# Kernel tuning notes

Hardware: AMD Instinct MI355X
Metric: run time of the kernel (lower is better)

The kernel has to match this reference:

```python
import jax, jax.numpy as jnp
import numpy as np

NUM_CLASSES = 80
NUM_CONVS = 4
SCORE_T = 0.05
TOPK = 1000
NMS_T = 0.6
MAX_DET = 100
STRIDES = (8, 16, 32, 64, 128)
LVL_HW = ((128, 168), (64, 84), (32, 42), (16, 21), (8, 11))
IMG_H, IMG_W = 1024, 1344
SCALE_CLAMP = float(np.log(1000.0 / 16.0))


def _conv(x, w, b):
    # x: (N,C,H,W), w: (O,I,3,3) -> same-padded 3x3 conv
    y = jax.lax.conv_general_dilated(x, w, (1, 1), 'SAME',
                                     dimension_numbers=('NCHW', 'OIHW', 'NCHW'))
    return y + b[None, :, None, None]


def _anchors(h, w, stride):
    # one anchor per location, size 4*stride, centered at pixel centers
    ys = (jnp.arange(h, dtype=jnp.float32) + 0.5) * stride
    xs = (jnp.arange(w, dtype=jnp.float32) + 0.5) * stride
    cy, cx = jnp.meshgrid(ys, xs, indexing='ij')
    cx, cy = cx.reshape(-1), cy.reshape(-1)
    half = 2.0 * stride
    return jnp.stack([cx - half, cy - half, cx + half, cy + half], -1)  # (HW,4)


def _decode(anchors, deltas):
    # Box2BoxTransform.apply_deltas with weights (1,1,1,1) + clip to image
    wa = anchors[..., 2] - anchors[..., 0]
    ha = anchors[..., 3] - anchors[..., 1]
    cxa = anchors[..., 0] + 0.5 * wa
    cya = anchors[..., 1] + 0.5 * ha
    dx, dy, dw, dh = (deltas[..., i] for i in range(4))
    dw = jnp.minimum(dw, SCALE_CLAMP)
    dh = jnp.minimum(dh, SCALE_CLAMP)
    cx = dx * wa + cxa
    cy = dy * ha + cya
    w = jnp.exp(dw) * wa
    h = jnp.exp(dh) * ha
    x1 = jnp.clip(cx - 0.5 * w, 0.0, IMG_W)
    y1 = jnp.clip(cy - 0.5 * h, 0.0, IMG_H)
    x2 = jnp.clip(cx + 0.5 * w, 0.0, IMG_W)
    y2 = jnp.clip(cy + 0.5 * h, 0.0, IMG_H)
    return jnp.stack([x1, y1, x2, y2], -1)


def _nms_single(boxes, scores, classes):
    # class-aware greedy NMS (batched_nms via per-class coordinate offset)
    M = boxes.shape[0]
    b = boxes + (classes.astype(boxes.dtype) * 2000.0)[:, None]
    order = jnp.argsort(-scores)
    b = b[order]
    s = scores[order]
    areas = (b[:, 2] - b[:, 0]) * (b[:, 3] - b[:, 1])
    idx = jnp.arange(M)

    def body(i, keep):
        bi = b[i]
        xx1 = jnp.maximum(bi[0], b[:, 0])
        yy1 = jnp.maximum(bi[1], b[:, 1])
        xx2 = jnp.minimum(bi[2], b[:, 2])
        yy2 = jnp.minimum(bi[3], b[:, 3])
        inter = jnp.clip(xx2 - xx1, 0.0) * jnp.clip(yy2 - yy1, 0.0)
        iou = inter / (areas[i] + areas - inter + 1e-9)
        sup = (iou > NMS_T) & (idx > i)
        alive = keep[i] & (s[i] > 0)
        return jnp.where(alive, keep & ~sup, keep)

    keep = jax.lax.fori_loop(0, M, body, jnp.ones((M,), bool))
    topv, topi = jax.lax.top_k(jnp.where(keep, s, 0.0), MAX_DET)
    sel = order[topi]
    return boxes[sel], topv, classes[sel]


def _forward(feat0, feat1, feat2, feat3, feat4, cls_w, cls_b, box_w, box_b,
             score_w, score_b, pred_w, pred_b, ctr_w, ctr_b):
    feats = [feat0, feat1, feat2, feat3, feat4]
    all_boxes, all_scores, all_classes = [], [], []
    for lvl, f in enumerate(feats):
        N = f.shape[0]
        x = f
        for i in range(NUM_CONVS):
            x = jax.nn.relu(_conv(x, cls_w[i], cls_b[i]))
        logits = _conv(x, score_w, score_b)          # (N,80,H,W)
        ctr = _conv(x, ctr_w, ctr_b)                 # (N,1,H,W)
        y = f
        for i in range(NUM_CONVS):
            y = jax.nn.relu(_conv(y, box_w[i], box_b[i]))
        deltas = _conv(y, pred_w, pred_b)            # (N,4,H,W)
        # permute_to_N_HWA_K
        logits = logits.transpose(0, 2, 3, 1).reshape(N, -1, NUM_CLASSES)
        deltas = deltas.transpose(0, 2, 3, 1).reshape(N, -1, 4)
        ctr = ctr.transpose(0, 2, 3, 1).reshape(N, -1, 1)
        scores = jnp.sqrt(jax.nn.sigmoid(logits) * jax.nn.sigmoid(ctr))
        flat = scores.reshape(N, -1)                 # (N, HW*K)
        k = min(TOPK, flat.shape[1])
        topv, topi = jax.lax.top_k(flat, k)
        topv = jnp.where(topv > SCORE_T, topv, 0.0)  # score threshold
        aidx = topi // NUM_CLASSES
        cidx = topi % NUM_CLASSES
        d = jnp.take_along_axis(deltas, aidx[..., None], axis=1)  # (N,k,4)
        h, w = LVL_HW[lvl]
        anc = _anchors(h, w, STRIDES[lvl])[aidx]     # (N,k,4)
        all_boxes.append(_decode(anc, d))
        all_scores.append(topv)
        all_classes.append(cidx)
    boxes = jnp.concatenate(all_boxes, 1)
    scores = jnp.concatenate(all_scores, 1)
    classes = jnp.concatenate(all_classes, 1)
    return jax.vmap(_nms_single)(boxes, scores, classes)


def setup_inputs() -> dict:
    key = jax.random.key(0)
    ks = jax.random.split(key, 10)
    d = {}
    shapes = {'feat0': (2, 256, 128, 168), 'feat1': (2, 256, 64, 84),
              'feat2': (2, 256, 32, 42), 'feat3': (2, 256, 16, 21),
              'feat4': (2, 256, 8, 11)}
    for i, (n, s) in enumerate(shapes.items()):
        d[n] = jax.random.normal(ks[i], s, dtype=jnp.float32)
    d['cls_w'] = jax.random.normal(ks[5], (4, 256, 256, 3, 3), jnp.float32) * 0.01
    d['cls_b'] = jnp.zeros((4, 256), jnp.float32)
    d['box_w'] = jax.random.normal(ks[6], (4, 256, 256, 3, 3), jnp.float32) * 0.01
    d['box_b'] = jnp.zeros((4, 256), jnp.float32)
    d['score_w'] = jax.random.normal(ks[7], (80, 256, 3, 3), jnp.float32) * 0.01
    d['score_b'] = jnp.full((80,), -float(np.log((1 - 0.01) / 0.01)), jnp.float32)
    d['pred_w'] = jax.random.normal(ks[8], (4, 256, 3, 3), jnp.float32) * 0.01
    d['pred_b'] = jnp.zeros((4,), jnp.float32)
    d['ctr_w'] = jax.random.normal(ks[9], (1, 256, 3, 3), jnp.float32) * 0.01
    d['ctr_b'] = jnp.zeros((1,), jnp.float32)
    return d


def reference(feat0, feat1, feat2, feat3, feat4, cls_w, cls_b, box_w, box_b,
              score_w, score_b, pred_w, pred_b, ctr_w, ctr_b):
    # returns (pred_boxes (N,100,4), scores (N,100), pred_classes (N,100))
    return _forward(feat0, feat1, feat2, feat3, feat4, cls_w, cls_b, box_w,
                    box_b, score_w, score_b, pred_w, pred_b, ctr_w, ctr_b)
```

## Files before the change

kernel.cpp:

```cpp
#include <hip/hip_runtime.h>
#include <math.h>

#define NCLS 80
#define KTOP 1000
#define SCORE_T 0.05f
#define NMS_T 0.6f
#define SCALE_CLAMP 4.135166556742356f
#define IMGW 1344.0f
#define IMGH 1024.0f

struct MCfg {
    const float* feat[5];
    long offIn[5];
    long offOutA[5];
    long offOutB[5];
    int tileBase[6];
    int tilesX[5];
    int Hs[5];
    int Ws[5];
    int nLvl;
    int useFeats;
};

template<int RELU>
__global__ __launch_bounds__(256, 2)
void conv_g(MCfg cfg,
            const float* __restrict__ inA, const float* __restrict__ inB,
            const float* __restrict__ wA, const float* __restrict__ wB,
            const float* __restrict__ bA, const float* __restrict__ bB,
            float* __restrict__ outA, float* __restrict__ outB,
            int CoutA, int CoutB, int zA)
{
    __shared__ float sIn[2][8][10][20];
    const int tid = threadIdx.x;
    const int n   = blockIdx.y;
    const int z   = blockIdx.z;
    const bool isA = (z < zA);
    const float* wt   = isA ? wA : wB;
    const float* bias = isA ? bA : bB;
    const int Cout    = isA ? CoutA : CoutB;
    const int cout0   = (isA ? z : z - zA) * 64;

    int tile = blockIdx.x;
    int lvl = 0;
    while (lvl + 1 < cfg.nLvl && tile >= cfg.tileBase[lvl + 1]) ++lvl;
    int t = tile - cfg.tileBase[lvl];
    const int tX = cfg.tilesX[lvl];
    int ty = 0;
    while (t >= tX) { t -= tX; ++ty; }
    const int tx = t;
    const int H = cfg.Hs[lvl], W = cfg.Ws[lvl], HW = H * W;
    const float* inbase = cfg.useFeats ? cfg.feat[lvl]
                                       : ((isA ? inA : inB) + cfg.offIn[lvl]);
    const float* inN = inbase + (size_t)n * 256 * HW;
    float* outbase = isA ? (outA + cfg.offOutA[lvl]) : (outB + cfg.offOutB[lvl]);

    const int h0 = ty * 8, w0 = tx * 16;
    const int cell = tid & 15, cg = tid >> 4;
    const int pr = (cell >> 2) << 1;
    const int pc = (cell & 3) << 2;
    const int q = tid & 3, pp0 = tid >> 2;

    float acc[4][8];
#pragma unroll
    for (int a = 0; a < 4; ++a)
#pragma unroll
        for (int b = 0; b < 8; ++b) acc[a][b] = 0.f;

    float rIn[10];

    auto issue = [&](int ci0) {
#pragma unroll
        for (int it = 0; it < 2; ++it) {
            int p = pp0 + it * 64;
            if (p < 80) {
                int ci = p / 10, row = p - ci * 10;
                int gh = h0 + row - 1;
                const float* src = inN + (size_t)(ci0 + ci) * HW;
#pragma unroll
                for (int j = 0; j < 5; ++j) {
                    int col = q * 5 + j, gw = w0 + col - 1;
                    float v = 0.f;
                    if (col < 18 && (unsigned)gh < (unsigned)H && (unsigned)gw < (unsigned)W)
                        v = src[(long)gh * W + gw];
                    rIn[it * 5 + j] = v;
                }
            }
        }
    };
    auto commit = [&](int buf) {
#pragma unroll
        for (int it = 0; it < 2; ++it) {
            int p = pp0 + it * 64;
            if (p < 80) {
                int ci = p / 10, row = p - ci * 10;
#pragma unroll
                for (int j = 0; j < 5; ++j)
                    sIn[buf][ci][row][q * 5 + j] = rIn[it * 5 + j];
            }
        }
    };

    const int cout_my = cout0 + cg * 4;

    issue(0);
    commit(0);
    __syncthreads();

    for (int r = 0; r < 32; ++r) {
        if (r < 31) issue((r + 1) * 8);
        const int cur = r & 1;
        const int cibase = r * 8;
#pragma unroll 2
        for (int ci = 0; ci < 8; ++ci) {
            float x[4][6];
#pragma unroll
            for (int rr = 0; rr < 4; ++rr)
#pragma unroll
                for (int c = 0; c < 6; ++c) x[rr][c] = sIn[cur][ci][pr + rr][pc + c];
#pragma unroll
            for (int cc = 0; cc < 4; ++cc) {
                int gc = cout_my + cc;
                int gcw = (gc < Cout) ? gc : 0;
                const float* wp = wt + ((size_t)gcw * 256 + (cibase + ci)) * 9;
                float4 wa = *(const float4*)(wp);
                float4 wb = *(const float4*)(wp + 4);
                float w8 = wp[8];
                float wv[9] = { wa.x, wa.y, wa.z, wa.w, wb.x, wb.y, wb.z, wb.w, w8 };
#pragma unroll
                for (int py = 0; py < 2; ++py)
#pragma unroll
                    for (int px = 0; px < 4; ++px) {
                        float s = acc[cc][py * 4 + px];
#pragma unroll
                        for (int dy = 0; dy < 3; ++dy)
#pragma unroll
                            for (int dx = 0; dx < 3; ++dx)
                                s = fmaf(wv[dy * 3 + dx], x[py + dy][px + dx], s);
                        acc[cc][py * 4 + px] = s;
                    }
            }
        }
        if (r < 31) commit((r + 1) & 1);
        __syncthreads();
    }

#pragma unroll
    for (int cc = 0; cc < 4; ++cc) {
        int gc = cout_my + cc;
        if (gc >= Cout) continue;
        float b = bias[gc];
        float* outc = outbase + ((size_t)n * Cout + gc) * HW;
#pragma unroll
        for (int py = 0; py < 2; ++py) {
            int gh = h0 + pr + py;
            if (gh >= H) continue;
#pragma unroll
            for (int px = 0; px < 4; ++px) {
                int gw = w0 + pc + px;
                if (gw >= W) continue;
                float v = acc[cc][py * 4 + px] + b;
                if (RELU) v = fmaxf(v, 0.f);
                outc[gh * W + gw] = v;
            }
        }
    }
}

__global__ void pack_kernel(const float* __restrict__ sw, const float* __restrict__ sb,
                            const float* __restrict__ cw, const float* __restrict__ cb,
                            float* __restrict__ pw, float* __restrict__ pb)
{
    int i = blockIdx.x * 256 + threadIdx.x;
    const int tot = 81 * 2304;
    if (i < tot) pw[i] = (i < 80 * 2304) ? sw[i] : cw[i - 80 * 2304];
    if (i < 81)  pb[i] = (i < 80) ? sb[i] : cb[i - 80];
}

struct LvlT {
    int HW[5]; int W[5]; float stride[5];
    long off81[5]; long offD[5];
};

__device__ inline float score_at(const float* __restrict__ L, int HW, int c, int pos)
{
    float l = L[(size_t)c * HW + pos];
    float ct = L[(size_t)80 * HW + pos];
    float sl = 1.f / (1.f + expf(-l));
    float sc = 1.f / (1.f + expf(-ct));
    return sqrtf(sl * sc);
}

__global__ __launch_bounds__(256)
void hist_b(LvlT T, const float* __restrict__ lg, unsigned* __restrict__ hist,
            const int* __restrict__ sel, int pass)
{
    __shared__ unsigned h[4096];
    int n = blockIdx.y, lvl = blockIdx.z, g = lvl * 2 + n;
    int HW = T.HW[lvl];
    int nel = HW * 80;
    const float* L = lg + T.off81[lvl] + (size_t)n * 81 * HW;
    unsigned* Hh = hist + g * 4096;
    const int* SL = sel + g * 8;
    for (int i = threadIdx.x; i < 4096; i += 256) h[i] = 0;
    __syncthreads();
    unsigned b1 = 0, b2 = 0;
    if (pass >= 1) b1 = (unsigned)SL[0];
    if (pass == 2) b2 = (unsigned)SL[2];
    int stride = gridDim.x * 256;
    for (int i = blockIdx.x * 256 + threadIdx.x; i < nel; i += stride) {
        int c = i / HW, pos = i - c * HW;
        unsigned bits = __float_as_uint(score_at(L, HW, c, pos));
        if (pass == 0) atomicAdd(&h[bits >> 24], 1u);
        else if (pass == 1) { if ((bits >> 24) == b1) atomicAdd(&h[(bits >> 12) & 0xFFFu], 1u); }
        else { if ((bits >> 12) == ((b1 << 12) | b2)) atomicAdd(&h[bits & 0xFFFu], 1u); }
    }
    __syncthreads();
    for (int i = threadIdx.x; i < 4096; i += 256)
        if (h[i]) atomicAdd(&Hh[i], h[i]);
}

__global__ __launch_bounds__(1024)
void scan_b(const unsigned* __restrict__ hist, int* __restrict__ sel, int pass)
{
    __shared__ unsigned ps[1024];
    int g = blockIdx.x;
    const unsigned* H = hist + g * 4096;
    int* SL = sel + g * 8;
    int tid = threadIdx.x;
    unsigned s = 0;
    if (pass == 0) s = (tid < 256) ? H[tid] : 0u;
    else { for (int b = 0; b < 4; ++b) s += H[tid * 4 + b]; }
    ps[tid] = s;
    __syncthreads();
    if (tid == 0) {
        unsigned base = 0;
        if (pass == 1) base = (unsigned)SL[1];
        else if (pass == 2) base = (unsigned)SL[3];
        unsigned cum = base, prev = 0;
        int fb = -1;
        for (int t = 1023; t >= 0; --t) {
            if (cum + ps[t] >= (unsigned)KTOP) {
                if (pass == 0) { fb = t; prev = cum; }
                else {
                    for (int b = t * 4 + 3; b >= t * 4; --b) {
                        unsigned c = H[b];
                        if (cum + c >= (unsigned)KTOP) { fb = b; prev = cum; break; }
                        cum += c;
                    }
                }
                break;
            }
            cum += ps[t];
        }
        if (pass == 0) { SL[0] = fb; SL[1] = (int)prev; }
        else if (pass == 1) { SL[2] = fb; SL[3] = (int)prev; }
        else {
            unsigned T = (((unsigned)SL[0]) << 24) | (((unsigned)SL[2]) << 12) | (unsigned)fb;
            SL[4] = (int)T; SL[5] = KTOP - (int)prev; SL[6] = (int)prev;
        }
    }
}

__global__ __launch_bounds__(256)
void compact_b(LvlT T, const float* __restrict__ lg, const int* __restrict__ sel,
               int* __restrict__ candIdx, float* __restrict__ candScore,
               unsigned* __restrict__ eqList, int* __restrict__ counters)
{
    int n = blockIdx.y, lvl = blockIdx.z, g = lvl * 2 + n;
    int HW = T.HW[lvl];
    int nel = HW * 80;
    const float* L = lg + T.off81[lvl] + (size_t)n * 81 * HW;
    unsigned Tt = (unsigned)sel[g * 8 + 4];
    int* cnt = counters + g * 2;
    int stride = gridDim.x * 256;
    for (int i = blockIdx.x * 256 + threadIdx.x; i < nel; i += stride) {
        int c = i / HW, pos = i - c * HW;
        float v = score_at(L, HW, c, pos);
        unsigned bits = __float_as_uint(v);
        int flat = pos * 80 + c;
        if (bits > Tt) {
            int s = atomicAdd(&cnt[0], 1);
            if (s < KTOP) {
                candIdx[n * 5000 + lvl * 1000 + s] = flat;
                candScore[n * 5000 + lvl * 1000 + s] = v;
            }
        } else if (bits == Tt) {
            int e = atomicAdd(&cnt[1], 1);
            if (e < 4096) eqList[g * 4096 + e] = (unsigned)flat;
        }
    }
}

template<typename T>
__device__ inline void bitonicSort(T* a, int N, bool desc)
{
    for (int k = 2; k <= N; k <<= 1)
        for (int j = k >> 1; j >= 1; j >>= 1) {
            for (int i = threadIdx.x; i < N; i += blockDim.x) {
                int l = i ^ j;
                if (l > i) {
                    T x = a[i], y = a[l];
                    bool up = ((i & k) == 0);
                    bool sw = desc ? (up ? (x < y) : (x > y)) : (up ? (x > y) : (x < y));
                    if (sw) { a[i] = y; a[l] = x; }
                }
            }
            __syncthreads();
        }
}

__global__ __launch_bounds__(256)
void eqfinish_b(const unsigned* __restrict__ eqList, const int* __restrict__ sel,
                const int* __restrict__ counters, int* __restrict__ candIdx,
                float* __restrict__ candScore)
{
    __shared__ unsigned L[4096];
    int g = blockIdx.x;
    int lvl = g >> 1, n = g & 1;
    int e = counters[g * 2 + 1]; if (e > 4096) e = 4096;
    int needEq = sel[g * 8 + 5];
    int base = sel[g * 8 + 6];
    unsigned T = (unsigned)sel[g * 8 + 4];
    for (int i = threadIdx.x; i < 4096; i += 256) L[i] = (i < e) ? eqList[g * 4096 + i] : 0xFFFFFFFFu;
    __syncthreads();
    bitonicSort(L, 4096, false);
    for (int t = threadIdx.x; t < needEq; t += 256) {
        int s = base + t;
        if (s < KTOP) {
            candIdx[n * 5000 + lvl * 1000 + s] = (int)L[t];
            candScore[n * 5000 + lvl * 1000 + s] = __uint_as_float(T);
        }
    }
}

__global__ __launch_bounds__(256)
void lvlsort_b(int* __restrict__ candIdx, float* __restrict__ candScore)
{
    __shared__ unsigned long long K[1024];
    int g = blockIdx.x;
    int lvl = g >> 1, n = g & 1;
    int* CI = candIdx + n * 5000 + lvl * 1000;
    float* CS = candScore + n * 5000 + lvl * 1000;
    for (int i = threadIdx.x; i < 1024; i += blockDim.x)
        K[i] = (i < KTOP)
             ? ((((unsigned long long)(unsigned)CI[i]) << 32) | __float_as_uint(CS[i]))
             : 0xFFFFFFFFFFFFFFFFULL;
    __syncthreads();
    bitonicSort(K, 1024, false);
    for (int i = threadIdx.x; i < KTOP; i += blockDim.x) {
        CI[i] = (int)(K[i] >> 32);
        CS[i] = __uint_as_float((unsigned)(K[i] & 0xFFFFFFFFu));
    }
}

__global__ __launch_bounds__(256)
void decode_b(LvlT T, const int* __restrict__ candIdx, const float* __restrict__ candScore,
              const float* __restrict__ deltas, float* __restrict__ candBox,
              float* __restrict__ candZ, int* __restrict__ candCls)
{
    int t = blockIdx.x * 256 + threadIdx.x;
    if (t >= 2 * 5000) return;
    int n = t / 5000, r = t % 5000;
    int lvl = r / 1000;
    int HW = T.HW[lvl], W = T.W[lvl];
    float stride = T.stride[lvl];
    int g = n * 5000 + r;
    int idx = candIdx[g];
    float raw = candScore[g];
    int pos = idx / NCLS, cls = idx % NCLS;
    int hh = pos / W, ww = pos % W;
    float cxa0 = ((float)ww + 0.5f) * stride;
    float cya0 = ((float)hh + 0.5f) * stride;
    float half = 2.f * stride;
    float a0 = cxa0 - half, a1 = cya0 - half, a2 = cxa0 + half, a3 = cya0 + half;
    float wa = a2 - a0, ha = a3 - a1;
    float cxa = a0 + 0.5f * wa, cya = a1 + 0.5f * ha;
    const float* D = deltas + T.offD[lvl] + (size_t)n * 4 * HW;
    float dx = D[pos], dy = D[HW + pos], dw = D[2 * HW + pos], dh = D[3 * HW + pos];
    dw = fminf(dw, SCALE_CLAMP); dh = fminf(dh, SCALE_CLAMP);
    float cx = dx * wa + cxa, cy = dy * ha + cya;
    float w2 = expf(dw) * wa, h2 = expf(dh) * ha;
    float x1 = fminf(fmaxf(cx - 0.5f * w2, 0.f), IMGW);
    float y1 = fminf(fmaxf(cy - 0.5f * h2, 0.f), IMGH);
    float x2 = fminf(fmaxf(cx + 0.5f * w2, 0.f), IMGW);
    float y2 = fminf(fmaxf(cy + 0.5f * h2, 0.f), IMGH);
    candBox[g * 4 + 0] = x1; candBox[g * 4 + 1] = y1;
    candBox[g * 4 + 2] = x2; candBox[g * 4 + 3] = y2;
    candZ[g] = (raw > SCORE_T) ? raw : 0.f;
    candCls[g] = cls;
}

__global__ __launch_bounds__(1024)
void gsort_kernel(const float* __restrict__ candZ, const float* __restrict__ candBox,
                  const int* __restrict__ candCls, float* __restrict__ sBox,
                  float* __restrict__ sScore, float* __restrict__ sCls,
                  float* __restrict__ sOffB, float* __restrict__ sArea)
{
    __shared__ unsigned long long K[8192];
    int n = blockIdx.x;
    for (int i = threadIdx.x; i < 8192; i += 1024)
        K[i] = (i < 5000)
             ? ((((unsigned long long)__float_as_uint(candZ[n * 5000 + i])) << 16)
                | (unsigned long long)(65535 - i))
             : 0ULL;
    __syncthreads();
    bitonicSort(K, 8192, true);
    for (int r = threadIdx.x; r < 5000; r += 1024) {
        unsigned long long k = K[r];
        int g = 65535 - (int)(k & 0xFFFFULL);
        float s = __uint_as_float((unsigned)((k >> 16) & 0xFFFFFFFFULL));
        int cls = candCls[n * 5000 + g];
        float b0 = candBox[(n * 5000 + g) * 4 + 0];
        float b1 = candBox[(n * 5000 + g) * 4 + 1];
        float b2 = candBox[(n * 5000 + g) * 4 + 2];
        float b3 = candBox[(n * 5000 + g) * 4 + 3];
        size_t o = (size_t)n * 5000 + r;
        sBox[o * 4 + 0] = b0; sBox[o * 4 + 1] = b1; sBox[o * 4 + 2] = b2; sBox[o * 4 + 3] = b3;
        sScore[o] = s;
        sCls[o] = (float)cls;
        float off = (float)cls * 2000.0f;
        float o0 = b0 + off, o1 = b1 + off, o2 = b2 + off, o3 = b3 + off;
        sOffB[o * 4 + 0] = o0; sOffB[o * 4 + 1] = o1; sOffB[o * 4 + 2] = o2; sOffB[o * 4 + 3] = o3;
        sArea[o] = (o2 - o0) * (o3 - o1);
    }
}

__global__ __launch_bounds__(64)
void nms_mask_kernel(const float* __restrict__ sOffB, const float* __restrict__ sArea,
                     unsigned long long* __restrict__ masks)
{
    __shared__ float jb0[64], jb1[64], jb2[64], jb3[64], ja[64];
    int jw = blockIdx.x;
    int it = blockIdx.y;
    int n  = blockIdx.z;
    int t = threadIdx.x;
    int jj = jw * 64 + t;
    const float* B = sOffB + (size_t)n * 5000 * 4;
    const float* A = sArea + (size_t)n * 5000;
    if (jj < 5000) {
        jb0[t] = B[jj * 4]; jb1[t] = B[jj * 4 + 1];
        jb2[t] = B[jj * 4 + 2]; jb3[t] = B[jj * 4 + 3];
        ja[t] = A[jj];
    } else {
        jb0[t] = -3e8f; jb1[t] = -3e8f; jb2[t] = -3e8f; jb3[t] = -3e8f; ja[t] = 0.f;
    }
    __syncthreads();
    int i = it * 64 + t;
    if (i >= 5000) return;
    float b0 = B[i * 4], b1 = B[i * 4 + 1], b2 = B[i * 4 + 2], b3 = B[i * 4 + 3];
    float ai = A[i];
    unsigned long long m = 0;
    for (int u = 0; u < 64; ++u) {
        float xx1 = fmaxf(b0, jb0[u]);
        float yy1 = fmaxf(b1, jb1[u]);
        float xx2 = fminf(b2, jb2[u]);
        float yy2 = fminf(b3, jb3[u]);
        float iw = fmaxf(xx2 - xx1, 0.f), ih = fmaxf(yy2 - yy1, 0.f);
        float inter = iw * ih;
        float iou = inter / (ai + ja[u] - inter + 1e-9f);
        if (iou > NMS_T) m |= (1ull << u);
    }
    masks[((size_t)n * 5000 + i) * 79 + jw] = m;
}

__global__ __launch_bounds__(128)
void nms_scan_kernel(const unsigned long long* __restrict__ masks,
                     const float* __restrict__ sScore, const float* __restrict__ sBox,
                     const float* __restrict__ sCls, float* __restrict__ out)
{
    __shared__ unsigned long long rem[80];
    __shared__ int alive[100], dead[100];
    __shared__ int st[3];
    int n = blockIdx.x, t = threadIdx.x;
    const float* S = sScore + (size_t)n * 5000;
    for (int i = t; i < 80; i += 128) rem[i] = 0ull;
    if (t == 0) { st[0] = 0; st[1] = 0; }
    __syncthreads();
    for (int i = 0; i < 5000; ++i) {
        if (t == 0) {
            bool sup = (rem[i >> 6] >> (i & 63)) & 1ull;
            float s = S[i];
            bool al = (!sup) && (s > 0.f);
            st[2] = al ? 1 : 0;
            if (al) { if (st[0] < 100) alive[st[0]] = i; st[0]++; }
            else    { if (st[1] < 100) dead[st[1]] = i;  st[1]++; }
        }
        __syncthreads();
        bool stop = (st[0] >= 100);
        if (st[2] && !stop) {
            const unsigned long long* row = masks + ((size_t)n * 5000 + i) * 79;
            if (t < 79) rem[t] |= row[t];
        }
        __syncthreads();
        if (stop) break;
    }
    __syncthreads();
    int na = st[0]; if (na > 100) na = 100;
    for (int r = t; r < 100; r += 128) {
        int p; float sc;
        if (r < na) { p = alive[r]; sc = S[p]; }
        else { p = dead[r - na]; sc = 0.f; }
        const float* bb = sBox + (((size_t)n * 5000) + p) * 4;
        out[(n * 100 + r) * 4 + 0] = bb[0];
        out[(n * 100 + r) * 4 + 1] = bb[1];
        out[(n * 100 + r) * 4 + 2] = bb[2];
        out[(n * 100 + r) * 4 + 3] = bb[3];
        out[800 + n * 100 + r] = sc;
        out[1000 + n * 100 + r] = sCls[(size_t)n * 5000 + p];
    }
}

extern "C" void kernel_launch(void* const* d_in, const int* in_sizes, int n_in,
                              void* d_out, int out_size, void* d_ws, size_t ws_size,
                              hipStream_t stream)
{
    const float* feat[5] = { (const float*)d_in[0], (const float*)d_in[1],
                             (const float*)d_in[2], (const float*)d_in[3],
                             (const float*)d_in[4] };
    const float* cls_w   = (const float*)d_in[5];
    const float* cls_b   = (const float*)d_in[6];
    const float* box_w   = (const float*)d_in[7];
    const float* box_b   = (const float*)d_in[8];
    const float* score_w = (const float*)d_in[9];
    const float* score_b = (const float*)d_in[10];
    const float* pred_w  = (const float*)d_in[11];
    const float* pred_b  = (const float*)d_in[12];
    const float* ctr_w   = (const float*)d_in[13];
    const float* ctr_b   = (const float*)d_in[14];

    char* ws = (char*)d_ws;
    size_t off = 0;
    auto alloc = [&](size_t nbytes) -> void* {
        void* p = ws + off;
        off += (nbytes + 255) & ~(size_t)255;
        return p;
    };
    const int   LH[5]  = { 128, 64, 32, 16, 8 };
    const int   LW[5]  = { 168, 84, 42, 21, 11 };
    const float LS[5]  = { 8.f, 16.f, 32.f, 64.f, 128.f };
    const int   LHW[5] = { 21504, 5376, 1344, 336, 88 };
    long off81[5], offD[5];
    { long a = 0, d = 0;
      for (int l = 0; l < 5; ++l) { off81[l] = a; offD[l] = d; a += 2L * 81 * LHW[l]; d += 2L * 4 * LHW[l]; } }
    long off256_14[4];
    { long a = 0; for (int l = 0; l < 4; ++l) { off256_14[l] = a; a += 2L * 256 * LHW[l + 1]; } }

    float* lg81   = (float*)alloc(sizeof(float) * (off81[4] + 2L * 81 * LHW[4]));
    float* deltas = (float*)alloc(sizeof(float) * (offD[4] + 2L * 4 * LHW[4]));
    float* packw  = (float*)alloc(sizeof(float) * 81 * 2304);
    float* packb  = (float*)alloc(sizeof(float) * 128);
    unsigned* hist = (unsigned*)alloc(sizeof(unsigned) * 10 * 4096);
    int* sel       = (int*)alloc(sizeof(int) * 10 * 8);
    int* counters  = (int*)alloc(sizeof(int) * 10 * 2);
    unsigned* eqList = (unsigned*)alloc(sizeof(unsigned) * 10 * 4096);
    int* candIdx     = (int*)alloc(sizeof(int) * 2 * 5000);
    float* candScore = (float*)alloc(sizeof(float) * 2 * 5000);
    float* candZ     = (float*)alloc(sizeof(float) * 2 * 5000);
    float* candBox   = (float*)alloc(sizeof(float) * 2 * 5000 * 4);
    int* candCls     = (int*)alloc(sizeof(int) * 2 * 5000);
    float* sBox   = (float*)alloc(sizeof(float) * 2 * 5000 * 4);
    float* sScore = (float*)alloc(sizeof(float) * 2 * 5000);
    float* sCls   = (float*)alloc(sizeof(float) * 2 * 5000);
    float* sOffB  = (float*)alloc(sizeof(float) * 2 * 5000 * 4);
    float* sArea  = (float*)alloc(sizeof(float) * 2 * 5000);

    const size_t bigE = 2L * 256 * LHW[0];
    const size_t bigB = sizeof(float) * bigE;
    bool wide = (ws_size >= off + 4 * (bigB + 256) + (1u << 20));

    float* clsP = (float*)alloc(bigB);
    float* clsQ = (float*)alloc(bigB);
    float* boxP = wide ? (float*)alloc(bigB) : clsP;
    float* boxQ = wide ? (float*)alloc(bigB) : clsQ;
    unsigned long long* masks = (unsigned long long*)clsP;

    pack_kernel<<<(81 * 2304 + 255) / 256, 256, 0, stream>>>(score_w, score_b, ctr_w, ctr_b, packw, packb);

    const size_t WS = 589824;

    MCfg c0{}, c0f{}, c0h{}, c14{}, c14f{}, c14h{};
    c0.feat[0] = feat[0];
    c0.tileBase[0] = 0; c0.tileBase[1] = 176;
    c0.tilesX[0] = 11; c0.Hs[0] = 128; c0.Ws[0] = 168;
    c0.nLvl = 1; c0.useFeats = 0;
    c0f = c0; c0f.useFeats = 1;
    c0h = c0;
    for (int l = 0; l < 4; ++l) {
        c14.feat[l] = feat[l + 1];
        c14.offIn[l] = off256_14[l];
        c14.offOutA[l] = off256_14[l];
        c14.offOutB[l] = off256_14[l];
        c14.tilesX[l] = (LW[l + 1] + 15) / 16;
        c14.Hs[l] = LH[l + 1]; c14.Ws[l] = LW[l + 1];
    }
    c14.tileBase[0] = 0; c14.tileBase[1] = 48; c14.tileBase[2] = 60;
    c14.tileBase[3] = 64; c14.tileBase[4] = 65;
    c14.nLvl = 4; c14.useFeats = 0;
    c14f = c14; c14f.useFeats = 1;
    c14h = c14;
    for (int l = 0; l < 4; ++l) { c14h.offOutA[l] = off81[l + 1]; c14h.offOutB[l] = offD[l + 1]; }

    if (wide) {
        dim3 gT(176, 2, 8), gH(176, 2, 3);
        conv_g<1><<<gT, 256, 0, stream>>>(c0f, feat[0], feat[0], cls_w + 0 * WS, box_w + 0 * WS, cls_b + 0,   box_b + 0,   clsP, boxP, 256, 256, 4);
        conv_g<1><<<gT, 256, 0, stream>>>(c0,  clsP,    boxP,    cls_w + 1 * WS, box_w + 1 * WS, cls_b + 256, box_b + 256, clsQ, boxQ, 256, 256, 4);
        conv_g<1><<<gT, 256, 0, stream>>>(c0,  clsQ,    boxQ,    cls_w + 2 * WS, box_w + 2 * WS, cls_b + 512, box_b + 512, clsP, boxP, 256, 256, 4);
        conv_g<1><<<gT, 256, 0, stream>>>(c0,  clsP,    boxP,    cls_w + 3 * WS, box_w + 3 * WS, cls_b + 768, box_b + 768, clsQ, boxQ, 256, 256, 4);
        conv_g<0><<<gH, 256, 0, stream>>>(c0h, clsQ,    boxQ,    packw,          pred_w,         packb,       pred_b,      lg81, deltas, 81, 4, 2);
        dim3 gT2(65, 2, 8), gH2(65, 2, 3);
        conv_g<1><<<gT2, 256, 0, stream>>>(c14f, feat[1], feat[1], cls_w + 0 * WS, box_w + 0 * WS, cls_b + 0,   box_b + 0,   clsP, boxP, 256, 256, 4);
        conv_g<1><<<gT2, 256, 0, stream>>>(c14,  clsP,    boxP,    cls_w + 1 * WS, box_w + 1 * WS, cls_b + 256, box_b + 256, clsQ, boxQ, 256, 256, 4);
        conv_g<1><<<gT2, 256, 0, stream>>>(c14,  clsQ,    boxQ,    cls_w + 2 * WS, box_w + 2 * WS, cls_b + 512, box_b + 512, clsP, boxP, 256, 256, 4);
        conv_g<1><<<gT2, 256, 0, stream>>>(c14,  clsP,    boxP,    cls_w + 3 * WS, box_w + 3 * WS, cls_b + 768, box_b + 768, clsQ, boxQ, 256, 256, 4);
        conv_g<0><<<gH2, 256, 0, stream>>>(c14h, clsQ,    boxQ,    packw,          pred_w,         packb,       pred_b,      lg81, deltas, 81, 4, 2);
    } else {
        dim3 gT(176, 2, 4), gHL(176, 2, 2), gHP(176, 2, 1);
        MCfg c0hL = c0, c0hP = c0;
        conv_g<1><<<gT, 256, 0, stream>>>(c0f, feat[0], feat[0], cls_w + 0 * WS, cls_w, cls_b + 0,   cls_b, clsP, clsP, 256, 256, 4);
        conv_g<1><<<gT, 256, 0, stream>>>(c0,  clsP,    clsP,    cls_w + 1 * WS, cls_w, cls_b + 256, cls_b, clsQ, clsQ, 256, 256, 4);
        conv_g<1><<<gT, 256, 0, stream>>>(c0,  clsQ,    clsQ,    cls_w + 2 * WS, cls_w, cls_b + 512, cls_b, clsP, clsP, 256, 256, 4);
        conv_g<1><<<gT, 256, 0, stream>>>(c0,  clsP,    clsP,    cls_w + 3 * WS, cls_w, cls_b + 768, cls_b, clsQ, clsQ, 256, 256, 4);
        conv_g<0><<<gHL, 256, 0, stream>>>(c0hL, clsQ,  clsQ,    packw,          packw, packb,       packb, lg81, lg81, 81, 81, 2);
        conv_g<1><<<gT, 256, 0, stream>>>(c0f, feat[0], feat[0], box_w + 0 * WS, box_w, box_b + 0,   box_b, clsP, clsP, 256, 256, 4);
        conv_g<1><<<gT, 256, 0, stream>>>(c0,  clsP,    clsP,    box_w + 1 * WS, box_w, box_b + 256, box_b, clsQ, clsQ, 256, 256, 4);
        conv_g<1><<<gT, 256, 0, stream>>>(c0,  clsQ,    clsQ,    box_w + 2 * WS, box_w, box_b + 512, box_b, clsP, clsP, 256, 256, 4);
        conv_g<1><<<gT, 256, 0, stream>>>(c0,  clsP,    clsP,    box_w + 3 * WS, box_w, box_b + 768, box_b, clsQ, clsQ, 256, 256, 4);
        conv_g<0><<<gHP, 256, 0, stream>>>(c0hP, clsQ,  clsQ,    pred_w,         pred_w, pred_b,     pred_b, deltas, deltas, 4, 4, 1);
        dim3 gT2(65, 2, 4), gHL2(65, 2, 2), gHP2(65, 2, 1);
        MCfg c14hL = c14h, c14hP = c14h;
        for (int l = 0; l < 4; ++l) { c14hP.offOutA[l] = offD[l + 1]; }
        conv_g<1><<<gT2, 256, 0, stream>>>(c14f, feat[1], feat[1], cls_w + 0 * WS, cls_w, cls_b + 0,   cls_b, clsP, clsP, 256, 256, 4);
        conv_g<1><<<gT2, 256, 0, stream>>>(c14,  clsP,    clsP,    cls_w + 1 * WS, cls_w, cls_b + 256, cls_b, clsQ, clsQ, 256, 256, 4);
        conv_g<1><<<gT2, 256, 0, stream>>>(c14,  clsQ,    clsQ,    cls_w + 2 * WS, cls_w, cls_b + 512, cls_b, clsP, clsP, 256, 256, 4);
        conv_g<1><<<gT2, 256, 0, stream>>>(c14,  clsP,    clsP,    cls_w + 3 * WS, cls_w, cls_b + 768, cls_b, clsQ, clsQ, 256, 256, 4);
        conv_g<0><<<gHL2, 256, 0, stream>>>(c14hL, clsQ, clsQ,    packw,          packw, packb,       packb, lg81, lg81, 81, 81, 2);
        conv_g<1><<<gT2, 256, 0, stream>>>(c14f, feat[1], feat[1], box_w + 0 * WS, box_w, box_b + 0,   box_b, clsP, clsP, 256, 256, 4);
        conv_g<1><<<gT2, 256, 0, stream>>>(c14,  clsP,    clsP,    box_w + 1 * WS, box_w, box_b + 256, box_b, clsQ, clsQ, 256, 256, 4);
        conv_g<1><<<gT2, 256, 0, stream>>>(c14,  clsQ,    clsQ,    box_w + 2 * WS, box_w, box_b + 512, box_b, clsP, clsP, 256, 256, 4);
        conv_g<1><<<gT2, 256, 0, stream>>>(c14,  clsP,    clsP,    box_w + 3 * WS, box_w, box_b + 768, box_b, clsQ, clsQ, 256, 256, 4);
        conv_g<0><<<gHP2, 256, 0, stream>>>(c14hP, clsQ, clsQ,    pred_w,         pred_w, pred_b,     pred_b, deltas, deltas, 4, 4, 1);
    }

    LvlT T{};
    for (int l = 0; l < 5; ++l) {
        T.HW[l] = LHW[l]; T.W[l] = LW[l]; T.stride[l] = LS[l];
        T.off81[l] = off81[l]; T.offD[l] = offD[l];
    }
    dim3 gHist(128, 2, 5);
    hipMemsetAsync(hist, 0, 10 * 4096 * sizeof(unsigned), stream);
    hist_b<<<gHist, 256, 0, stream>>>(T, lg81, hist, sel, 0);
    scan_b<<<10, 1024, 0, stream>>>(hist, sel, 0);
    hipMemsetAsync(hist, 0, 10 * 4096 * sizeof(unsigned), stream);
    hist_b<<<gHist, 256, 0, stream>>>(T, lg81, hist, sel, 1);
    scan_b<<<10, 1024, 0, stream>>>(hist, sel, 1);
    hipMemsetAsync(hist, 0, 10 * 4096 * sizeof(unsigned), stream);
    hist_b<<<gHist, 256, 0, stream>>>(T, lg81, hist, sel, 2);
    scan_b<<<10, 1024, 0, stream>>>(hist, sel, 2);
    hipMemsetAsync(counters, 0, 10 * 2 * sizeof(int), stream);
    compact_b<<<gHist, 256, 0, stream>>>(T, lg81, sel, candIdx, candScore, eqList, counters);
    eqfinish_b<<<10, 256, 0, stream>>>(eqList, sel, counters, candIdx, candScore);
    lvlsort_b<<<10, 256, 0, stream>>>(candIdx, candScore);
    decode_b<<<(2 * 5000 + 255) / 256, 256, 0, stream>>>(T, candIdx, candScore, deltas,
                                                         candBox, candZ, candCls);
    gsort_kernel<<<2, 1024, 0, stream>>>(candZ, candBox, candCls, sBox, sScore, sCls, sOffB, sArea);
    dim3 gM(79, 79, 2);
    nms_mask_kernel<<<gM, 64, 0, stream>>>(sOffB, sArea, masks);
    nms_scan_kernel<<<2, 128, 0, stream>>>(masks, sScore, sBox, sCls, (float*)d_out);
}
```

Baseline: 10.00 ms.

## Restructure 3x3 conv with wave-uniform packed weights, larger tiles and fused heads

Replaces the conv kernel with a variant that uses 16x16 spatial tiles and up to 1024 threads per block. Each wave owns four output channels, so its weight reads are wave-uniform (readfirstlane) and can come from scalar loads. Weights are repacked once into a 12-float-aligned layout so each tap group loads as two float4 plus one scalar. The class-logit, centerness and box-delta heads are merged into one packed 96-channel head launch. The aim is to cut per-lane weight traffic and launch count, at the cost of fewer accumulators per thread, a larger shared-memory footprint and an extra repack pass over the tower weights.

```diff
diff --git a/kernel.cpp b/kernel.cpp
--- a/kernel.cpp
+++ b/kernel.cpp
@@ -22,24 +22,23 @@
     int useFeats;
 };
 
-template<int RELU>
-__global__ __launch_bounds__(256, 2)
-void conv_g(MCfg cfg,
+template<int NW, int HEAD>
+__global__ __launch_bounds__(NW * 64)
+void conv_s(MCfg cfg,
             const float* __restrict__ inA, const float* __restrict__ inB,
-            const float* __restrict__ wA, const float* __restrict__ wB,
-            const float* __restrict__ bA, const float* __restrict__ bB,
-            float* __restrict__ outA, float* __restrict__ outB,
-            int CoutA, int CoutB, int zA)
-{
-    __shared__ float sIn[2][8][10][20];
+            const float* __restrict__ wpkA, const float* __restrict__ wpkB,
+            const float* __restrict__ biasA, const float* __restrict__ biasB,
+            float* __restrict__ outA, float* __restrict__ outB, int zA)
+{
+    __shared__ float sIn[2][8][18][20];
     const int tid = threadIdx.x;
     const int n   = blockIdx.y;
     const int z   = blockIdx.z;
     const bool isA = (z < zA);
-    const float* wt   = isA ? wA : wB;
-    const float* bias = isA ? bA : bB;
-    const int Cout    = isA ? CoutA : CoutB;
-    const int cout0   = (isA ? z : z - zA) * 64;
+    const float* wpk  = isA ? wpkA : wpkB;
+    const float* bias = isA ? biasA : biasB;
+    const int cbase = HEAD ? (isA ? z * 16 : 80)
+                           : (isA ? z : z - zA) * 64;
 
     int tile = blockIdx.x;
     int lvl = 0;
@@ -53,128 +52,174 @@
     const float* inbase = cfg.useFeats ? cfg.feat[lvl]
                                        : ((isA ? inA : inB) + cfg.offIn[lvl]);
     const float* inN = inbase + (size_t)n * 256 * HW;
-    float* outbase = isA ? (outA + cfg.offOutA[lvl]) : (outB + cfg.offOutB[lvl]);
-
-    const int h0 = ty * 8, w0 = tx * 16;
-    const int cell = tid & 15, cg = tid >> 4;
-    const int pr = (cell >> 2) << 1;
-    const int pc = (cell & 3) << 2;
-    const int q = tid & 3, pp0 = tid >> 2;
-
-    float acc[4][8];
+
+    const int h0 = ty * 16, w0 = tx * 16;
+    const int wv  = __builtin_amdgcn_readfirstlane(tid >> 6);
+    const int gc0 = cbase + wv * 4;
+    const float* wb = wpk + (size_t)gc0 * 3072;
+    const int lane = tid & 63;
+    const int pr = (lane >> 3) << 1;
+    const int pc = (lane & 7) << 1;
+
+    float acc[4][4];
 #pragma unroll
     for (int a = 0; a < 4; ++a)
 #pragma unroll
-        for (int b = 0; b < 8; ++b) acc[a][b] = 0.f;
-
-    float rIn[10];
+        for (int b = 0; b < 4; ++b) acc[a][b] = 0.f;
+
+    constexpr int NTHR = NW * 64;
+    constexpr int NIT = (2592 + NTHR - 1) / NTHR;
+    float rIn[NIT];
 
     auto issue = [&](int ci0) {
 #pragma unroll
-        for (int it = 0; it < 2; ++it) {
-            int p = pp0 + it * 64;
-            if (p < 80) {
-                int ci = p / 10, row = p - ci * 10;
-                int gh = h0 + row - 1;
-                const float* src = inN + (size_t)(ci0 + ci) * HW;
-#pragma unroll
-                for (int j = 0; j < 5; ++j) {
-                    int col = q * 5 + j, gw = w0 + col - 1;
-                    float v = 0.f;
-                    if (col < 18 && (unsigned)gh < (unsigned)H && (unsigned)gw < (unsigned)W)
-                        v = src[(long)gh * W + gw];
-                    rIn[it * 5 + j] = v;
-                }
+        for (int it = 0; it < NIT; ++it) {
+            int idx = it * NTHR + tid;
+            float v = 0.f;
+            if (idx < 2592) {
+                int ci = idx / 324, rm = idx - ci * 324;
+                int row = rm / 18, col = rm - row * 18;
+                int gh = h0 + row - 1, gw = w0 + col - 1;
+                if ((unsigned)gh < (unsigned)H && (unsigned)gw < (unsigned)W)
+                    v = inN[(size_t)(ci0 + ci) * HW + (long)gh * W + gw];
             }
+            rIn[it] = v;
         }
     };
     auto commit = [&](int buf) {
 #pragma unroll
-        for (int it = 0; it < 2; ++it) {
-            int p = pp0 + it * 64;
-            if (p < 80) {
-                int ci = p / 10, row = p - ci * 10;
-#pragma unroll
-                for (int j = 0; j < 5; ++j)
-                    sIn[buf][ci][row][q * 5 + j] = rIn[it * 5 + j];
+        for (int it = 0; it < NIT; ++it) {
+            int idx = it * NTHR + tid;
+            if (idx < 2592) {
+                int ci = idx / 324, rm = idx - ci * 324;
+                int row = rm / 18, col = rm - row * 18;
+                sIn[buf][ci][row][col] = rIn[it];
             }
         }
     };
-
-    const int cout_my = cout0 + cg * 4;
 
     issue(0);
     commit(0);
     __syncthreads();
 
-    for (int r = 0; r < 32; ++r) {
-        if (r < 31) issue((r + 1) * 8);
-        const int cur = r & 1;
-        const int cibase = r * 8;
-#pragma unroll 2
+    for (int rs = 0; rs < 32; ++rs) {
+        if (rs < 31) issue((rs + 1) * 8);
+        const float (*S)[18][20] = sIn[rs & 1];
+        const int cib = rs * 8;
+#pragma unroll
         for (int ci = 0; ci < 8; ++ci) {
-            float x[4][6];
-#pragma unroll
-            for (int rr = 0; rr < 4; ++rr)
-#pragma unroll
-                for (int c = 0; c < 6; ++c) x[rr][c] = sIn[cur][ci][pr + rr][pc + c];
+            float x[4][4];
+#pragma unroll
+            for (int i = 0; i < 4; ++i) {
+                float2 u0 = *(const float2*)&S[ci][pr + i][pc];
+                float2 u1 = *(const float2*)&S[ci][pr + i][pc + 2];
+                x[i][0] = u0.x; x[i][1] = u0.y; x[i][2] = u1.x; x[i][3] = u1.y;
+            }
 #pragma unroll
             for (int cc = 0; cc < 4; ++cc) {
-                int gc = cout_my + cc;
-                int gcw = (gc < Cout) ? gc : 0;
-                const float* wp = wt + ((size_t)gcw * 256 + (cibase + ci)) * 9;
-                float4 wa = *(const float4*)(wp);
-                float4 wb = *(const float4*)(wp + 4);
-                float w8 = wp[8];
-                float wv[9] = { wa.x, wa.y, wa.z, wa.w, wb.x, wb.y, wb.z, wb.w, w8 };
+                const float* wp = wb + cc * 3072 + (size_t)(cib + ci) * 12;
+                float4 qa = *(const float4*)wp;
+                float4 qb = *(const float4*)(wp + 4);
+                float q8 = wp[8];
+                float wv9[9] = { qa.x, qa.y, qa.z, qa.w, qb.x, qb.y, qb.z, qb.w, q8 };
 #pragma unroll
                 for (int py = 0; py < 2; ++py)
 #pragma unroll
-                    for (int px = 0; px < 4; ++px) {
-                        float s = acc[cc][py * 4 + px];
+                    for (int px = 0; px < 2; ++px) {
+                        float s = acc[cc][py * 2 + px];
 #pragma unroll
                         for (int dy = 0; dy < 3; ++dy)
 #pragma unroll
                             for (int dx = 0; dx < 3; ++dx)
-                                s = fmaf(wv[dy * 3 + dx], x[py + dy][px + dx], s);
-                        acc[cc][py * 4 + px] = s;
+                                s = fmaf(wv9[dy * 3 + dx], x[py + dy][px + dx], s);
+                        acc[cc][py * 2 + px] = s;
                     }
             }
         }
-        if (r < 31) commit((r + 1) & 1);
+        if (rs < 31) commit((rs + 1) & 1);
         __syncthreads();
     }
 
 #pragma unroll
     for (int cc = 0; cc < 4; ++cc) {
-        int gc = cout_my + cc;
-        if (gc >= Cout) continue;
+        int gc = gc0 + cc;
+        if (HEAD) {
+            if (isA) { if (gc >= 81) continue; }
+            else     { if (gc < 81 || gc >= 85) continue; }
+        }
         float b = bias[gc];
-        float* outc = outbase + ((size_t)n * Cout + gc) * HW;
+        float* outc;
+        if (!HEAD)
+            outc = (isA ? outA + cfg.offOutA[lvl] : outB + cfg.offOutB[lvl])
+                 + ((size_t)n * 256 + gc) * HW;
+        else if (isA)
+            outc = outA + cfg.offOutA[lvl] + ((size_t)n * 81 + gc) * HW;
+        else
+            outc = outB + cfg.offOutB[lvl] + ((size_t)n * 4 + (gc - 81)) * HW;
 #pragma unroll
         for (int py = 0; py < 2; ++py) {
             int gh = h0 + pr + py;
             if (gh >= H) continue;
 #pragma unroll
-            for (int px = 0; px < 4; ++px) {
+            for (int px = 0; px < 2; ++px) {
                 int gw = w0 + pc + px;
                 if (gw >= W) continue;
-                float v = acc[cc][py * 4 + px] + b;
-                if (RELU) v = fmaxf(v, 0.f);
-                outc[gh * W + gw] = v;
+                float v = acc[cc][py * 2 + px] + b;
+                if (!HEAD) v = fmaxf(v, 0.f);
+                outc[(long)gh * W + gw] = v;
             }
         }
     }
 }
 
-__global__ void pack_kernel(const float* __restrict__ sw, const float* __restrict__ sb,
-                            const float* __restrict__ cw, const float* __restrict__ cb,
-                            float* __restrict__ pw, float* __restrict__ pb)
-{
+__global__ __launch_bounds__(256)
+void packT_kernel(const float* __restrict__ cw, const float* __restrict__ bw,
+                  float* __restrict__ dst)
+{
+    const long tot = 2L * 4 * 256 * 256 * 12;
+    long stride = (long)gridDim.x * 256;
+    for (long i = (long)blockIdx.x * 256 + threadIdx.x; i < tot; i += stride) {
+        int k = (int)(i % 12);
+        long r = i / 12;
+        int ci = (int)(r % 256); r /= 256;
+        int co = (int)(r % 256); r /= 256;
+        int layer = (int)(r % 4);
+        int tower = (int)(r / 4);
+        const float* src = tower ? bw : cw;
+        float v = (k < 9) ? src[(((size_t)layer * 256 + co) * 256 + ci) * 9 + k] : 0.f;
+        dst[i] = v;
+    }
+}
+
+__global__ __launch_bounds__(256)
+void packH_kernel(const float* __restrict__ sw, const float* __restrict__ sb,
+                  const float* __restrict__ cw, const float* __restrict__ cb,
+                  const float* __restrict__ pw, const float* __restrict__ pb,
+                  float* __restrict__ dst, float* __restrict__ dstb)
+{
+    const int tot = 96 * 256 * 12;
+    int stride = gridDim.x * 256;
+    for (int i = blockIdx.x * 256 + threadIdx.x; i < tot; i += stride) {
+        int k = i % 12;
+        int r = i / 12;
+        int ci = r % 256;
+        int co = r / 256;
+        float v = 0.f;
+        if (k < 9) {
+            if (co < 80)      v = sw[((size_t)co * 256 + ci) * 9 + k];
+            else if (co == 80) v = cw[(size_t)ci * 9 + k];
+            else if (co < 85)  v = pw[((size_t)(co - 81) * 256 + ci) * 9 + k];
+        }
+        dst[i] = v;
+    }
     int i = blockIdx.x * 256 + threadIdx.x;
-    const int tot = 81 * 2304;
-    if (i < tot) pw[i] = (i < 80 * 2304) ? sw[i] : cw[i - 80 * 2304];
-    if (i < 81)  pb[i] = (i < 80) ? sb[i] : cb[i - 80];
+    if (i < 96) {
+        float v = 0.f;
+        if (i < 80) v = sb[i];
+        else if (i == 80) v = cb[0];
+        else if (i < 85) v = pb[i - 81];
+        dstb[i] = v;
+    }
 }
 
 struct LvlT {
@@ -546,10 +591,12 @@
     long off256_14[4];
     { long a = 0; for (int l = 0; l < 4; ++l) { off256_14[l] = a; a += 2L * 256 * LHW[l + 1]; } }
 
+    const long LSTRIDE = 256L * 256 * 12;
+    float* packT  = (float*)alloc(sizeof(float) * 2 * 4 * LSTRIDE);
+    float* packH  = (float*)alloc(sizeof(float) * 96 * 256 * 12);
+    float* packHb = (float*)alloc(sizeof(float) * 96);
     float* lg81   = (float*)alloc(sizeof(float) * (off81[4] + 2L * 81 * LHW[4]));
     float* deltas = (float*)alloc(sizeof(float) * (offD[4] + 2L * 4 * LHW[4]));
-    float* packw  = (float*)alloc(sizeof(float) * 81 * 2304);
-    float* packb  = (float*)alloc(sizeof(float) * 128);
     unsigned* hist = (unsigned*)alloc(sizeof(unsigned) * 10 * 4096);
     int* sel       = (int*)alloc(sizeof(int) * 10 * 8);
     int* counters  = (int*)alloc(sizeof(int) * 10 * 2);
@@ -565,9 +612,9 @@
     float* sOffB  = (float*)alloc(sizeof(float) * 2 * 5000 * 4);
     float* sArea  = (float*)alloc(sizeof(float) * 2 * 5000);
 
-    const size_t bigE = 2L * 256 * LHW[0];
-    const size_t bigB = sizeof(float) * bigE;
-    bool wide = (ws_size >= off + 4 * (bigB + 256) + (1u << 20));
+    const size_t bigB = sizeof(float) * 2L * 256 * LHW[0];
+    const size_t bigPad = (bigB + 255) & ~(size_t)255;
+    bool wide = (ws_size >= off + 4 * bigPad + (1u << 20));
 
     float* clsP = (float*)alloc(bigB);
     float* clsQ = (float*)alloc(bigB);
@@ -575,17 +622,19 @@
     float* boxQ = wide ? (float*)alloc(bigB) : clsQ;
     unsigned long long* masks = (unsigned long long*)clsP;
 
-    pack_kernel<<<(81 * 2304 + 255) / 256, 256, 0, stream>>>(score_w, score_b, ctr_w, ctr_b, packw, packb);
-
-    const size_t WS = 589824;
-
-    MCfg c0{}, c0f{}, c0h{}, c14{}, c14f{}, c14h{};
+    const float* pkC = packT;
+    const float* pkB = packT + 4 * LSTRIDE;
+
+    packT_kernel<<<2048, 256, 0, stream>>>(cls_w, box_w, packT);
+    packH_kernel<<<1152, 256, 0, stream>>>(score_w, score_b, ctr_w, ctr_b,
+                                           pred_w, pred_b, packH, packHb);
+
+    MCfg c0{}, c0f{}, c14{}, c14f{}, c14h{};
     c0.feat[0] = feat[0];
-    c0.tileBase[0] = 0; c0.tileBase[1] = 176;
+    c0.tileBase[0] = 0; c0.tileBase[1] = 88;
     c0.tilesX[0] = 11; c0.Hs[0] = 128; c0.Ws[0] = 168;
     c0.nLvl = 1; c0.useFeats = 0;
     c0f = c0; c0f.useFeats = 1;
-    c0h = c0;
     for (int l = 0; l < 4; ++l) {
         c14.feat[l] = feat[l + 1];
         c14.offIn[l] = off256_14[l];
@@ -594,52 +643,50 @@
         c14.tilesX[l] = (LW[l + 1] + 15) / 16;
         c14.Hs[l] = LH[l + 1]; c14.Ws[l] = LW[l + 1];
     }
-    c14.tileBase[0] = 0; c14.tileBase[1] = 48; c14.tileBase[2] = 60;
-    c14.tileBase[3] = 64; c14.tileBase[4] = 65;
+    c14.tileBase[0] = 0; c14.tileBase[1] = 24; c14.tileBase[2] = 30;
+    c14.tileBase[3] = 32; c14.tileBase[4] = 33;
     c14.nLvl = 4; c14.useFeats = 0;
     c14f = c14; c14f.useFeats = 1;
     c14h = c14;
     for (int l = 0; l < 4; ++l) { c14h.offOutA[l] = off81[l + 1]; c14h.offOutB[l] = offD[l + 1]; }
 
     if (wide) {
-        dim3 gT(176, 2, 8), gH(176, 2, 3);
-        conv_g<1><<<gT, 256, 0, stream>>>(c0f, feat[0], feat[0], cls_w + 0 * WS, box_w + 0 * WS, cls_b + 0,   box_b + 0,   clsP, boxP, 256, 256, 4);
-        conv_g<1><<<gT, 256, 0, stream>>>(c0,  clsP,    boxP,    cls_w + 1 * WS, box_w + 1 * WS, cls_b + 256, box_b + 256, clsQ, boxQ, 256, 256, 4);
-        conv_g<1><<<gT, 256, 0, stream>>>(c0,  clsQ,    boxQ,    cls_w + 2 * WS, box_w + 2 * WS, cls_b + 512, box_b + 512, clsP, boxP, 256, 256, 4);
-        conv_g<1><<<gT, 256, 0, stream>>>(c0,  clsP,    boxP,    cls_w + 3 * WS, box_w + 3 * WS, cls_b + 768, box_b + 768, clsQ, boxQ, 256, 256, 4);
-        conv_g<0><<<gH, 256, 0, stream>>>(c0h, clsQ,    boxQ,    packw,          pred_w,         packb,       pred_b,      lg81, deltas, 81, 4, 2);
-        dim3 gT2(65, 2, 8), gH2(65, 2, 3);
-        conv_g<1><<<gT2, 256, 0, stream>>>(c14f, feat[1], feat[1], cls_w + 0 * WS, box_w + 0 * WS, cls_b + 0,   box_b + 0,   clsP, boxP, 256, 256, 4);
-        conv_g<1><<<gT2, 256, 0, stream>>>(c14,  clsP,    boxP,    cls_w + 1 * WS, box_w + 1 * WS, cls_b + 256, box_b + 256, clsQ, boxQ, 256, 256, 4);
-        conv_g<1><<<gT2, 256, 0, stream>>>(c14,  clsQ,    boxQ,    cls_w + 2 * WS, box_w + 2 * WS, cls_b + 512, box_b + 512, clsP, boxP, 256, 256, 4);
-        conv_g<1><<<gT2, 256, 0, stream>>>(c14,  clsP,    boxP,    cls_w + 3 * WS, box_w + 3 * WS, cls_b + 768, box_b + 768, clsQ, boxQ, 256, 256, 4);
-        conv_g<0><<<gH2, 256, 0, stream>>>(c14h, clsQ,    boxQ,    packw,          pred_w,         packb,       pred_b,      lg81, deltas, 81, 4, 2);
+        dim3 gM0(88, 2, 8), gH0(88, 2, 7);
+        conv_s<16,0><<<gM0, 1024, 0, stream>>>(c0f, feat[0], feat[0], pkC + 0*LSTRIDE, pkB + 0*LSTRIDE, cls_b + 0,   box_b + 0,   clsP, boxP, 4);
+        conv_s<16,0><<<gM0, 1024, 0, stream>>>(c0,  clsP,    boxP,    pkC + 1*LSTRIDE, pkB + 1*LSTRIDE, cls_b + 256, box_b + 256, clsQ, boxQ, 4);
+        conv_s<16,0><<<gM0, 1024, 0, stream>>>(c0,  clsQ,    boxQ,    pkC + 2*LSTRIDE, pkB + 2*LSTRIDE, cls_b + 512, box_b + 512, clsP, boxP, 4);
+        conv_s<16,0><<<gM0, 1024, 0, stream>>>(c0,  clsP,    boxP,    pkC + 3*LSTRIDE, pkB + 3*LSTRIDE, cls_b + 768, box_b + 768, clsQ, boxQ, 4);
+        conv_s<4,1><<<gH0, 256, 0, stream>>>(c0,  clsQ,    boxQ,    packH, packH, packHb, packHb, lg81, deltas, 6);
+
+        dim3 gM1(33, 2, 8), gH1(33, 2, 7);
+        conv_s<16,0><<<gM1, 1024, 0, stream>>>(c14f, feat[1], feat[1], pkC + 0*LSTRIDE, pkB + 0*LSTRIDE, cls_b + 0,   box_b + 0,   clsP, boxP, 4);
+        conv_s<16,0><<<gM1, 1024, 0, stream>>>(c14,  clsP,    boxP,    pkC + 1*LSTRIDE, pkB + 1*LSTRIDE, cls_b + 256, box_b + 256, clsQ, boxQ, 4);
+        conv_s<16,0><<<gM1, 1024, 0, stream>>>(c14,  clsQ,    boxQ,    pkC + 2*LSTRIDE, pkB + 2*LSTRIDE, cls_b + 512, box_b + 512, clsP, boxP, 4);
+        conv_s<16,0><<<gM1, 1024, 0, stream>>>(c14,  clsP,    boxP,    pkC + 3*LSTRIDE, pkB + 3*LSTRIDE, cls_b + 768, box_b + 768, clsQ, boxQ, 4);
+        conv_s<4,1><<<gH1, 256, 0, stream>>>(c14h, clsQ,    boxQ,    packH, packH, packHb, packHb, lg81, deltas, 6);
     } else {
-        dim3 gT(176, 2, 4), gHL(176, 2, 2), gHP(176, 2, 1);
-        MCfg c0hL = c0, c0hP = c0;
-        conv_g<1><<<gT, 256, 0, stream>>>(c0f, feat[0], feat[0], cls_w + 0 * WS, cls_w, cls_b + 0,   cls_b, clsP, clsP, 256, 256, 4);
-        conv_g<1><<<gT, 256, 0, stream>>>(c0,  clsP,    clsP,    cls_w + 1 * WS, cls_w, cls_b + 256, cls_b, clsQ, clsQ, 256, 256, 4);
-        conv_g<1><<<gT, 256, 0, stream>>>(c0,  clsQ,    clsQ,    cls_w + 2 * WS, cls_w, cls_b + 512, cls_b, clsP, clsP, 256, 256, 4);
-        conv_g<1><<<gT, 256, 0, stream>>>(c0,  clsP,    clsP,    cls_w + 3 * WS, cls_w, cls_b + 768, cls_b, clsQ, clsQ, 256, 256, 4);
-        conv_g<0><<<gHL, 256, 0, stream>>>(c0hL, clsQ,  clsQ,    packw,          packw, packb,       packb, lg81, lg81, 81, 81, 2);
-        conv_g<1><<<gT, 256, 0, stream>>>(c0f, feat[0], feat[0], box_w + 0 * WS, box_w, box_b + 0,   box_b, clsP, clsP, 256, 256, 4);
-        conv_g<1><<<gT, 256, 0, stream>>>(c0,  clsP,    clsP,    box_w + 1 * WS, box_w, box_b + 256, box_b, clsQ, clsQ, 256, 256, 4);
-        conv_g<1><<<gT, 256, 0, stream>>>(c0,  clsQ,    clsQ,    box_w + 2 * WS, box_w, box_b + 512, box_b, clsP, clsP, 256, 256, 4);
-        conv_g<1><<<gT, 256, 0, stream>>>(c0,  clsP,    clsP,    box_w + 3 * WS, box_w, box_b + 768, box_b, clsQ, clsQ, 256, 256, 4);
-        conv_g<0><<<gHP, 256, 0, stream>>>(c0hP, clsQ,  clsQ,    pred_w,         pred_w, pred_b,     pred_b, deltas, deltas, 4, 4, 1);
-        dim3 gT2(65, 2, 4), gHL2(65, 2, 2), gHP2(65, 2, 1);
-        MCfg c14hL = c14h, c14hP = c14h;
-        for (int l = 0; l < 4; ++l) { c14hP.offOutA[l] = offD[l + 1]; }
-        conv_g<1><<<gT2, 256, 0, stream>>>(c14f, feat[1], feat[1], cls_w + 0 * WS, cls_w, cls_b + 0,   cls_b, clsP, clsP, 256, 256, 4);
-        conv_g<1><<<gT2, 256, 0, stream>>>(c14,  clsP,    clsP,    cls_w + 1 * WS, cls_w, cls_b + 256, cls_b, clsQ, clsQ, 256, 256, 4);
-        conv_g<1><<<gT2, 256, 0, stream>>>(c14,  clsQ,    clsQ,    cls_w + 2 * WS, cls_w, cls_b + 512, cls_b, clsP, clsP, 256, 256, 4);
-        conv_g<1><<<gT2, 256, 0, stream>>>(c14,  clsP,    clsP,    cls_w + 3 * WS, cls_w, cls_b + 768, cls_b, clsQ, clsQ, 256, 256, 4);
-        conv_g<0><<<gHL2, 256, 0, stream>>>(c14hL, clsQ, clsQ,    packw,          packw, packb,       packb, lg81, lg81, 81, 81, 2);
-        conv_g<1><<<gT2, 256, 0, stream>>>(c14f, feat[1], feat[1], box_w + 0 * WS, box_w, box_b + 0,   box_b, clsP, clsP, 256, 256, 4);
-        conv_g<1><<<gT2, 256, 0, stream>>>(c14,  clsP,    clsP,    box_w + 1 * WS, box_w, box_b + 256, box_b, clsQ, clsQ, 256, 256, 4);
-        conv_g<1><<<gT2, 256, 0, stream>>>(c14,  clsQ,    clsQ,    box_w + 2 * WS, box_w, box_b + 512, box_b, clsP, clsP, 256, 256, 4);
-        conv_g<1><<<gT2, 256, 0, stream>>>(c14,  clsP,    clsP,    box_w + 3 * WS, box_w, box_b + 768, box_b, clsQ, clsQ, 256, 256, 4);
-        conv_g<0><<<gHP2, 256, 0, stream>>>(c14hP, clsQ, clsQ,    pred_w,         pred_w, pred_b,     pred_b, deltas, deltas, 4, 4, 1);
+        dim3 gM0(88, 2, 4), gHA0(88, 2, 6), gHB0(88, 2, 1);
+        conv_s<16,0><<<gM0, 1024, 0, stream>>>(c0f, feat[0], feat[0], pkC + 0*LSTRIDE, pkC, cls_b + 0,   cls_b, clsP, clsP, 4);
+        conv_s<16,0><<<gM0, 1024, 0, stream>>>(c0,  clsP,    clsP,    pkC + 1*LSTRIDE, pkC, cls_b + 256, cls_b, clsQ, clsQ, 4);
+        conv_s<16,0><<<gM0, 1024, 0, stream>>>(c0,  clsQ,    clsQ,    pkC + 2*LSTRIDE, pkC, cls_b + 512, cls_b, clsP, clsP, 4);
+        conv_s<16,0><<<gM0, 1024, 0, stream>>>(c0,  clsP,    clsP,    pkC + 3*LSTRIDE, pkC, cls_b + 768, cls_b, clsQ, clsQ, 4);
+        conv_s<4,1><<<gHA0, 256, 0, stream>>>(c0,  clsQ,    clsQ,    packH, packH, packHb, packHb, lg81, deltas, 6);
+        conv_s<16,0><<<gM0, 1024, 0, stream>>>(c0f, feat[0], feat[0], pkB + 0*LSTRIDE, pkB, box_b + 0,   box_b, clsP, clsP, 4);
+        conv_s<16,0><<<gM0, 1024, 0, stream>>>(c0,  clsP,    clsP,    pkB + 1*LSTRIDE, pkB, box_b + 256, box_b, clsQ, clsQ, 4);
+        conv_s<16,0><<<gM0, 1024, 0, stream>>>(c0,  clsQ,    clsQ,    pkB + 2*LSTRIDE, pkB, box_b + 512, box_b, clsP, clsP, 4);
+        conv_s<16,0><<<gM0, 1024, 0, stream>>>(c0,  clsP,    clsP,    pkB + 3*LSTRIDE, pkB, box_b + 768, box_b, clsQ, clsQ, 4);
+        conv_s<4,1><<<gHB0, 256, 0, stream>>>(c0,  clsQ,    clsQ,    packH, packH, packHb, packHb, lg81, deltas, 0);
+        dim3 gM1(33, 2, 4), gHA1(33, 2, 6), gHB1(33, 2, 1);
+        conv_s<16,0><<<gM1, 1024, 0, stream>>>(c14f, feat[1], feat[1], pkC + 0*LSTRIDE, pkC, cls_b + 0,   cls_b, clsP, clsP, 4);
+        conv_s<16,0><<<gM1, 1024, 0, stream>>>(c14,  clsP,    clsP,    pkC + 1*LSTRIDE, pkC, cls_b + 256, cls_b, clsQ, clsQ, 4);
+        conv_s<16,0><<<gM1, 1024, 0, stream>>>(c14,  clsQ,    clsQ,    pkC + 2*LSTRIDE, pkC, cls_b + 512, cls_b, clsP, clsP, 4);
+        conv_s<16,0><<<gM1, 1024, 0, stream>>>(c14,  clsP,    clsP,    pkC + 3*LSTRIDE, pkC, cls_b + 768, cls_b, clsQ, clsQ, 4);
+        conv_s<4,1><<<gHA1, 256, 0, stream>>>(c14h, clsQ,    clsQ,    packH, packH, packHb, packHb, lg81, deltas, 6);
+        conv_s<16,0><<<gM1, 1024, 0, stream>>>(c14f, feat[1], feat[1], pkB + 0*LSTRIDE, pkB, box_b + 0,   box_b, clsP, clsP, 4);
+        conv_s<16,0><<<gM1, 1024, 0, stream>>>(c14,  clsP,    clsP,    pkB + 1*LSTRIDE, pkB, box_b + 256, box_b, clsQ, clsQ, 4);
+        conv_s<16,0><<<gM1, 1024, 0, stream>>>(c14,  clsQ,    clsQ,    pkB + 2*LSTRIDE, pkB, box_b + 512, box_b, clsP, clsP, 4);
+        conv_s<16,0><<<gM1, 1024, 0, stream>>>(c14,  clsP,    clsP,    pkB + 3*LSTRIDE, pkB, box_b + 768, box_b, clsQ, clsQ, 4);
+        conv_s<4,1><<<gHB1, 256, 0, stream>>>(c14h, clsQ,    clsQ,    packH, packH, packHb, packHb, lg81, deltas, 0);
     }
 
     LvlT T{};
```

New measurement: 28.88 ms. 189% more time.
